# Kernel tuning notes

Hardware: AMD Instinct MI355X
Metric: run time of the kernel (lower is better)

The kernel has to match this reference:

```python
import jax, jax.numpy as jnp
import numpy as np

B, S, F = 256, 512, 26
H, M, C = 512, 256, 20  # rnn_hidden, mlp_hidden, num_classes


def setup_inputs() -> dict:
    key = jax.random.key(0)
    ks = jax.random.split(key, 9)
    s_ih = 1.0 / np.sqrt(H)
    return {
        "x": jax.random.normal(ks[0], (B, S, F), dtype=jnp.float32),
        "w_ih": jax.random.uniform(ks[1], (4 * H, F), jnp.float32, -s_ih, s_ih),
        "w_hh": jax.random.uniform(ks[2], (4 * H, H), jnp.float32, -s_ih, s_ih),
        "b_ih": jax.random.uniform(ks[3], (4 * H,), jnp.float32, -s_ih, s_ih),
        "b_hh": jax.random.uniform(ks[4], (4 * H,), jnp.float32, -s_ih, s_ih),
        "w1": jax.random.uniform(ks[5], (M, H), jnp.float32, -s_ih, s_ih),
        "b1": jax.random.uniform(ks[6], (M,), jnp.float32, -s_ih, s_ih),
        "w2": jax.random.uniform(ks[7], (C, M), jnp.float32, -1.0 / np.sqrt(M), 1.0 / np.sqrt(M)),
        "b2": jax.random.uniform(ks[8], (C,), jnp.float32, -1.0 / np.sqrt(M), 1.0 / np.sqrt(M)),
    }


def reference(x, w_ih, w_hh, b_ih, b_hh, w1, b1, w2, b2):
    b, s, _ = x.shape
    h0 = jnp.zeros((b, H), x.dtype)
    c0 = jnp.zeros((b, H), x.dtype)
    bias = b_ih + b_hh

    def step(carry, xt):
        h, c = carry
        # original stores hx.data -> state carried into next step is detached
        h = jax.lax.stop_gradient(h)
        c = jax.lax.stop_gradient(c)
        z = xt @ w_ih.T + h @ w_hh.T + bias  # [b, 4H]
        i, f, g, o = jnp.split(z, 4, axis=-1)  # PyTorch gate order i,f,g,o
        c2 = jax.nn.sigmoid(f) * c + jax.nn.sigmoid(i) * jnp.tanh(g)
        h2 = jax.nn.sigmoid(o) * jnp.tanh(c2)
        return (h2, c2), h2

    _, hs = jax.lax.scan(step, (h0, c0), jnp.transpose(x, (1, 0, 2)))  # hs: [s, b, H]
    hs = jnp.transpose(hs, (1, 0, 2))  # [b, s, H]
    hidden = jax.nn.relu(jnp.einsum("bsh,mh->bsm", hs, w1) + b1)
    logits = jnp.einsum("bsm,cm->bsc", hidden, w2) + b2
    return jax.nn.log_softmax(logits, axis=-1)
```

## Files before the change

kernel.cpp:

```cpp
#include <hip/hip_runtime.h>

#define S_LEN 512
#define HID   512
#define FEAT  26
#define NCLS  20
#define DRING 16

typedef short bf16x8 __attribute__((ext_vector_type(8)));
typedef float f32x4  __attribute__((ext_vector_type(4)));

__device__ __forceinline__ unsigned short f2bf(float f) {
    unsigned u = __builtin_bit_cast(unsigned, f);
    unsigned r = (u + 0x7FFFu + ((u >> 16) & 1u)) >> 16;
    return (unsigned short)r;
}
__device__ __forceinline__ float sigm(float x) { return 1.f / (1.f + __expf(-x)); }
__device__ __forceinline__ float tanh_f(float x) {
    float xc = fminf(fmaxf(x, -15.f), 15.f);
    float t = __expf(-2.f * xc);
    return (1.f - t) / (1.f + t);
}

__device__ __forceinline__ void load4_coherent(const unsigned short* p,
                                               uint4& a0, uint4& a1, uint4& a2, uint4& a3) {
    asm volatile(
        "global_load_dwordx4 %0, %4, off sc0 sc1\n\t"
        "global_load_dwordx4 %1, %5, off sc0 sc1\n\t"
        "global_load_dwordx4 %2, %6, off sc0 sc1\n\t"
        "global_load_dwordx4 %3, %7, off sc0 sc1\n\t"
        "s_waitcnt vmcnt(0)"
        : "=&v"(a0), "=&v"(a1), "=&v"(a2), "=&v"(a3)
        : "v"(p), "v"(p + 8), "v"(p + 16), "v"(p + 24)
        : "memory");
}
__device__ __forceinline__ void store_coherent(unsigned short* p, unsigned d) {
    asm volatile(
        "global_store_dword %0, %1, off sc0 sc1\n\t"
        "s_waitcnt vmcnt(0)"
        :: "v"(p), "v"(d) : "memory");
}
__device__ __forceinline__ void store_coherent_x2(unsigned short* p, unsigned long long d) {
    asm volatile(
        "global_store_dwordx2 %0, %1, off sc0 sc1\n\t"
        "s_waitcnt vmcnt(0)"
        :: "v"(p), "v"(d) : "memory");
}
__device__ __forceinline__ void store_u32_nowait(unsigned* p, unsigned d) {
    asm volatile("global_store_dword %0, %1, off sc0 sc1" :: "v"(p), "v"(d) : "memory");
}
__device__ __forceinline__ unsigned load_u32_coherent(const unsigned* p) {
    unsigned v;
    asm volatile("global_load_dword %0, %1, off sc0 sc1\n\ts_waitcnt vmcnt(0)"
                 : "=v"(v) : "v"(p) : "memory");
    return v;
}
__device__ __forceinline__ void store_u32_sys_wait(unsigned* p, unsigned d) {
    asm volatile("global_store_dword %0, %1, off sc0 sc1\n\ts_waitcnt vmcnt(0)"
                 :: "v"(p), "v"(d) : "memory");
}
__device__ __forceinline__ void load2_nw_sys(const unsigned short* p, uint4& a0, uint4& a1) {
    asm volatile(
        "global_load_dwordx4 %0, %2, off sc0 sc1\n\t"
        "global_load_dwordx4 %1, %3, off sc0 sc1"
        : "=&v"(a0), "=&v"(a1) : "v"(p), "v"(p + 8) : "memory");
}

__device__ __forceinline__ void load4_l2(const unsigned short* p,
                                         uint4& a0, uint4& a1, uint4& a2, uint4& a3) {
    asm volatile(
        "global_load_dwordx4 %0, %4, off sc0\n\t"
        "global_load_dwordx4 %1, %5, off sc0\n\t"
        "global_load_dwordx4 %2, %6, off sc0\n\t"
        "global_load_dwordx4 %3, %7, off sc0\n\t"
        "s_waitcnt vmcnt(0)"
        : "=&v"(a0), "=&v"(a1), "=&v"(a2), "=&v"(a3)
        : "v"(p), "v"(p + 8), "v"(p + 16), "v"(p + 24)
        : "memory");
}
__device__ __forceinline__ void store_l2_x2(unsigned short* p, unsigned long long d) {
    asm volatile(
        "global_store_dwordx2 %0, %1, off sc0\n\t"
        "s_waitcnt vmcnt(0)"
        :: "v"(p), "v"(d) : "memory");
}
__device__ __forceinline__ void store_u32_nowait_l2(unsigned* p, unsigned d) {
    asm volatile("global_store_dword %0, %1, off sc0" :: "v"(p), "v"(d) : "memory");
}
__device__ __forceinline__ unsigned load_u32_l2(const unsigned* p) {
    unsigned v;
    asm volatile("global_load_dword %0, %1, off sc0\n\ts_waitcnt vmcnt(0)"
                 : "=v"(v) : "v"(p) : "memory");
    return v;
}
__device__ __forceinline__ void load2_nw_l2(const unsigned short* p, uint4& a0, uint4& a1) {
    asm volatile(
        "global_load_dwordx4 %0, %2, off sc0\n\t"
        "global_load_dwordx4 %1, %3, off sc0"
        : "=&v"(a0), "=&v"(a1) : "v"(p), "v"(p + 8) : "memory");
}

__global__ void prep_kernel(const float* __restrict__ w1, const float* __restrict__ w2,
                            unsigned short* __restrict__ w1b, unsigned short* __restrict__ w2b,
                            unsigned* __restrict__ syncw, int nclear) {
    int i = blockIdx.x * 256 + threadIdx.x;
    if (i < nclear) syncw[i] = 0u;
    if (i < 256 * 512) w1b[i] = f2bf(w1[i]);
    if (i < NCLS * 256) w2b[i] = f2bf(w2[i]);
}

__global__ __launch_bounds__(256, 1) void lstm_big_kernel(
    const float* __restrict__ x,
    const float* __restrict__ w_ih,
    const float* __restrict__ w_hh,
    const float* __restrict__ b_ih,
    const float* __restrict__ b_hh,
    const unsigned short* __restrict__ w1b,
    const float* __restrict__ b1,
    const unsigned short* __restrict__ w2b,
    const float* __restrict__ b2,
    float* __restrict__ out,
    unsigned short* __restrict__ hs,
    unsigned* __restrict__ flags)
{
    const int tid  = threadIdx.x;
    const int wave = tid >> 6;
    const int lane = tid & 63;
    const int quad = lane >> 4;
    const int l16  = lane & 15;

    const int  bx      = blockIdx.x;
    const int  xasm    = bx & 7;
    const int  kslt    = bx >> 3;
    const bool is_lstm = (kslt < 16);
    const int  ksub    = is_lstm ? kslt : (kslt - 16);
    const int  clust   = xasm * 2 + (ksub >> 3);
    const int  sub     = ksub & 7;

    __shared__ __align__(16) unsigned short At[16 * 552];
    __shared__ __align__(16) unsigned short hid[16 * 264];
    __shared__ float lg[16 * 24];
    __shared__ unsigned rdy;
    __shared__ unsigned fastf;
    if (tid == 0) rdy = 0u;

    {
        unsigned xcc;
        asm volatile("s_getreg_b32 %0, hwreg(HW_REG_XCC_ID)" : "=s"(xcc));
        if (tid == 0) {
            unsigned* slot = flags + (clust * 8 + sub) * 16 + (is_lstm ? 8 : 9);
            store_u32_sys_wait(slot, (xcc & 0xFu) + 1u);
        }
        if (wave == 0) {
            const unsigned* ps = flags + (clust * 8 + (lane & 7)) * 16 + ((lane & 8) ? 9 : 8);
            unsigned myx = 1u;
            for (;;) {
                unsigned v = 1u;
                if (lane < 16) v = load_u32_coherent(ps);
                if (__ballot(v != 0u) == ~0ull) { myx = v; break; }
                __builtin_amdgcn_s_sleep(2);
            }
            unsigned ref = __shfl(myx, 0);
            bool eq = (lane >= 16) || (myx == ref);
            if (tid == 0) fastf = (__ballot(eq) == ~0ull) ? 1u : 0u;
        }
    }
    __syncthreads();
    const bool fast = (fastf != 0u);

    if (is_lstm) {
        const int wic = sub;
        const int B0  = clust * 16;
        const int U0  = wic * 64;

        bf16x8 bB[4][17];
#pragma unroll
        for (int g = 0; g < 4; ++g) {
            const int row = g * 512 + U0 + wave * 16 + l16;
            const float* wrow = w_hh + (size_t)row * HID;
#pragma unroll
            for (int kk = 0; kk < 16; ++kk) {
                const float* p = wrow + kk * 32 + quad * 8;
                bf16x8 v;
#pragma unroll
                for (int j = 0; j < 8; ++j) v[j] = (short)f2bf(p[j]);
                bB[g][kk] = v;
            }
            const float* irow = w_ih + (size_t)row * FEAT;
            bf16x8 v;
#pragma unroll
            for (int j = 0; j < 8; ++j) {
                int ftr = quad * 8 + j;
                v[j] = (ftr < FEAT) ? (short)f2bf(irow[ftr]) : (short)0;
            }
            bB[g][16] = v;
        }

        f32x4 biasv[4];
#pragma unroll
        for (int g = 0; g < 4; ++g)
#pragma unroll
            for (int r = 0; r < 4; ++r) {
                int rr = g * 512 + U0 + wave * 16 + quad * 4 + r;
                biasv[g][r] = b_ih[rr] + b_hh[rr];
            }
        float cst[4] = {0.f, 0.f, 0.f, 0.f};

        const int sm = tid >> 4;
        const int sc = tid & 15;
        unsigned short* hsc = hs + (size_t)clust * S_LEN * 16 * HID;
        unsigned* myflag = flags + (clust * 8 + wic) * 16;
        const unsigned* peer = flags + (clust * 8 + (lane & 7)) * 16;

        for (int t = 0; t < S_LEN; ++t) {
            {
                unsigned pk = 0u;
                if (sc <= 12) {
                    float2 xv = *(const float2*)(x + ((size_t)(B0 + sm) * S_LEN + t) * FEAT + sc * 2);
                    pk = (unsigned)f2bf(xv.x) | ((unsigned)f2bf(xv.y) << 16);
                }
                *(unsigned*)(At + sm * 552 + 512 + sc * 2) = pk;
            }

            f32x4 acc[4];
#pragma unroll
            for (int g = 0; g < 4; ++g) acc[g] = biasv[g];

            if (t > 0) {
                const unsigned tt = (unsigned)t;
                unsigned long long bal;
                for (;;) {
                    unsigned v = ~0u;
                    if (lane < 8) v = fast ? load_u32_l2(peer) : load_u32_coherent(peer);
                    bal = __ballot(v >= tt);
                    if ((bal & 0xFull) == 0xFull) break;
                    if (!fast) __builtin_amdgcn_s_sleep(1);
                }
                const bool g1ok = ((bal >> 4) & 0xFull) == 0xFull;

                const unsigned short* srow = hsc + ((size_t)(t - 1) * 16 + sm) * HID;
                uint4 s0, s1, s2, s3;
                if (fast) load2_nw_l2(srow + sc * 16, s0, s1);
                else      load2_nw_sys(srow + sc * 16, s0, s1);

                if (!g1ok) {
                    for (;;) {
                        unsigned v = ~0u;
                        if (lane >= 4 && lane < 8)
                            v = fast ? load_u32_l2(peer) : load_u32_coherent(peer);
                        unsigned long long b2_ = __ballot(v >= tt);
                        if (((b2_ >> 4) & 0xFull) == 0xFull) break;
                        if (!fast) __builtin_amdgcn_s_sleep(1);
                    }
                }
                asm volatile("s_waitcnt vmcnt(0)" ::: "memory");
                __builtin_amdgcn_sched_barrier(0);
                {
                    unsigned short* dst = At + sm * 552 + sc * 16;
                    *(uint4*)(dst)     = s0;
                    *(uint4*)(dst + 8) = s1;
                }
                if (fast) load2_nw_l2(srow + 256 + sc * 16, s2, s3);
                else      load2_nw_sys(srow + 256 + sc * 16, s2, s3);

                asm volatile("s_waitcnt lgkmcnt(0)" ::: "memory");
                __builtin_amdgcn_sched_barrier(0);
                __builtin_amdgcn_s_barrier();

                const unsigned short* arow = At + l16 * 552 + quad * 8;
                {
                    bf16x8 hx = __builtin_bit_cast(bf16x8, *(const uint4*)(arow + 16 * 32));
#pragma unroll
                    for (int g = 0; g < 4; ++g)
                        acc[g] = __builtin_amdgcn_mfma_f32_16x16x32_bf16(bB[g][16], hx, acc[g], 0, 0, 0);
                }
#pragma unroll
                for (int kk = 0; kk < 8; ++kk) {
                    bf16x8 h = __builtin_bit_cast(bf16x8, *(const uint4*)(arow + kk * 32));
#pragma unroll
                    for (int g = 0; g < 4; ++g)
                        acc[g] = __builtin_amdgcn_mfma_f32_16x16x32_bf16(bB[g][kk], h, acc[g], 0, 0, 0);
                }

                asm volatile("s_waitcnt vmcnt(0)" ::: "memory");
                __builtin_amdgcn_sched_barrier(0);
                {
                    unsigned short* dst = At + sm * 552 + 256 + sc * 16;
                    *(uint4*)(dst)     = s2;
                    *(uint4*)(dst + 8) = s3;
                }
                asm volatile("s_waitcnt lgkmcnt(0)" ::: "memory");
                __builtin_amdgcn_sched_barrier(0);
                __builtin_amdgcn_s_barrier();

#pragma unroll
                for (int kk = 8; kk < 16; ++kk) {
                    bf16x8 h = __builtin_bit_cast(bf16x8, *(const uint4*)(arow + kk * 32));
#pragma unroll
                    for (int g = 0; g < 4; ++g)
                        acc[g] = __builtin_amdgcn_mfma_f32_16x16x32_bf16(bB[g][kk], h, acc[g], 0, 0, 0);
                }
            } else {
                __syncthreads();
                const unsigned short* arow = At + l16 * 552 + quad * 8;
                bf16x8 hx = __builtin_bit_cast(bf16x8, *(const uint4*)(arow + 16 * 32));
#pragma unroll
                for (int g = 0; g < 4; ++g)
                    acc[g] = __builtin_amdgcn_mfma_f32_16x16x32_bf16(bB[g][16], hx, acc[g], 0, 0, 0);
            }

            {
                unsigned short hv[4];
#pragma unroll
                for (int r = 0; r < 4; ++r) {
                    float cn = sigm(acc[1][r]) * cst[r] + sigm(acc[0][r]) * tanh_f(acc[2][r]);
                    cst[r] = cn;
                    hv[r] = f2bf(sigm(acc[3][r]) * tanh_f(cn));
                }
                unsigned long long d = (unsigned long long)hv[0]
                                     | ((unsigned long long)hv[1] << 16)
                                     | ((unsigned long long)hv[2] << 32)
                                     | ((unsigned long long)hv[3] << 48);
                unsigned short* hp = hsc + ((size_t)t * 16 + l16) * HID
                                   + U0 + wave * 16 + quad * 4;
                if (fast) store_l2_x2(hp, d);
                else      store_coherent_x2(hp, d);
            }
            __syncthreads();
            if (tid == 0) {
                if (fast) store_u32_nowait_l2(myflag, (unsigned)(t + 1));
                else      store_u32_nowait(myflag, (unsigned)(t + 1));
            }
        }
    } else {
        const int mc  = clust;
        const int m   = sub;
        const int B0  = mc * 16;
        const unsigned* peer = flags + (mc * 8 + (lane & 7)) * 16;
        const unsigned short* hsc = hs + (size_t)mc * S_LEN * 16 * HID;
        const int sm = tid >> 4;
        const int sc = tid & 15;

        for (int t = m; t < S_LEN; t += 8) {
            if (wave == 0) {
                for (;;) {
                    unsigned v = fast ? load_u32_l2(peer) : load_u32_coherent(peer);
                    if (__ballot(v >= (unsigned)(t + 1)) == ~0ull) break;
                    __builtin_amdgcn_s_sleep(8);
                }
                if (lane == 0)
                    __hip_atomic_store(&rdy, (unsigned)(t + 1), __ATOMIC_RELAXED,
                                       __HIP_MEMORY_SCOPE_WORKGROUP);
            } else {
                while (__hip_atomic_load(&rdy, __ATOMIC_RELAXED,
                                         __HIP_MEMORY_SCOPE_WORKGROUP) < (unsigned)(t + 1))
                    __builtin_amdgcn_s_sleep(8);
            }
            {
                const unsigned short* src = hsc + ((size_t)t * 16 + sm) * HID + sc * 32;
                unsigned short* dst = At + sm * 552 + sc * 32;
                uint4 a0, a1, a2, a3;
                if (fast) load4_l2(src, a0, a1, a2, a3);
                else      load4_coherent(src, a0, a1, a2, a3);
                *(uint4*)(dst)      = a0;
                *(uint4*)(dst + 8)  = a1;
                *(uint4*)(dst + 16) = a2;
                *(uint4*)(dst + 24) = a3;
            }
            __syncthreads();

            f32x4 a1[4];
#pragma unroll
            for (int nt = 0; nt < 4; ++nt) a1[nt] = (f32x4){0.f, 0.f, 0.f, 0.f};
#pragma unroll
            for (int kk = 0; kk < 16; ++kk) {
                bf16x8 a = __builtin_bit_cast(
                    bf16x8, *(const uint4*)(At + l16 * 552 + kk * 32 + quad * 8));
#pragma unroll
                for (int nt = 0; nt < 4; ++nt) {
                    int n = wave * 64 + nt * 16 + l16;
                    bf16x8 b = __builtin_bit_cast(
                        bf16x8, *(const uint4*)(w1b + (size_t)n * 512 + kk * 32 + quad * 8));
                    a1[nt] = __builtin_amdgcn_mfma_f32_16x16x32_bf16(a, b, a1[nt], 0, 0, 0);
                }
            }
#pragma unroll
            for (int nt = 0; nt < 4; ++nt) {
                int n = wave * 64 + nt * 16 + l16;
                float bv = b1[n];
#pragma unroll
                for (int r = 0; r < 4; ++r)
                    hid[(quad * 4 + r) * 264 + n] = f2bf(fmaxf(a1[nt][r] + bv, 0.f));
            }
            __syncthreads();
            if (wave == 0) {
                f32x4 a2[2];
                a2[0] = (f32x4){0.f, 0.f, 0.f, 0.f};
                a2[1] = (f32x4){0.f, 0.f, 0.f, 0.f};
#pragma unroll
                for (int kk = 0; kk < 8; ++kk) {
                    bf16x8 a = __builtin_bit_cast(
                        bf16x8, *(const uint4*)(hid + l16 * 264 + kk * 32 + quad * 8));
#pragma unroll
                    for (int nt = 0; nt < 2; ++nt) {
                        int n = nt * 16 + l16;
                        bf16x8 b;
                        if (n < NCLS) {
                            b = __builtin_bit_cast(
                                bf16x8, *(const uint4*)(w2b + (size_t)n * 256 + kk * 32 + quad * 8));
                        } else {
                            uint4 z; z.x = z.y = z.z = z.w = 0u;
                            b = __builtin_bit_cast(bf16x8, z);
                        }
                        a2[nt] = __builtin_amdgcn_mfma_f32_16x16x32_bf16(a, b, a2[nt], 0, 0, 0);
                    }
                }
#pragma unroll
                for (int nt = 0; nt < 2; ++nt) {
                    int n = nt * 16 + l16;
                    if (n < NCLS) {
                        float bv = b2[n];
#pragma unroll
                        for (int r = 0; r < 4; ++r)
                            lg[(quad * 4 + r) * 24 + n] = a2[nt][r] + bv;
                    }
                }
            }
            __syncthreads();
            if (tid < 16) {
                float v[NCLS];
                float mx = -3.4e38f;
#pragma unroll
                for (int c = 0; c < NCLS; ++c) { v[c] = lg[tid * 24 + c]; mx = fmaxf(mx, v[c]); }
                float s = 0.f;
#pragma unroll
                for (int c = 0; c < NCLS; ++c) s += __expf(v[c] - mx);
                float lse = mx + __logf(s);
                float* orow = out + ((size_t)(B0 + tid) * S_LEN + t) * NCLS;
#pragma unroll
                for (int c = 0; c < NCLS; ++c) orow[c] = v[c] - lse;
            }
            __syncthreads();
        }
    }
}

__global__ __launch_bounds__(256, 2) void lstm_fused_kernel(
    const float* __restrict__ x, const float* __restrict__ w_ih,
    const float* __restrict__ w_hh, const float* __restrict__ b_ih,
    const float* __restrict__ b_hh, const unsigned short* __restrict__ w1b,
    const float* __restrict__ b1, const unsigned short* __restrict__ w2b,
    const float* __restrict__ b2, float* __restrict__ out,
    unsigned short* __restrict__ hb, unsigned* __restrict__ flags,
    unsigned* __restrict__ done)
{
    const int tid  = threadIdx.x;
    const int wave = tid >> 6;
    const int lane = tid & 63;
    const int quad = lane >> 4;
    const int l16  = lane & 15;
    const int wg   = blockIdx.x;

    __shared__ __align__(16) unsigned short At[16 * 552];
    __shared__ float zb[16 * 132];
    __shared__ __align__(16) unsigned short hid[16 * 264];
    __shared__ float lg[16 * 24];
    __shared__ unsigned rdy;
    if (tid == 0) rdy = 0u;
    __syncthreads();

    if (wg < 256) {
        const int clust = (wg & 7) * 2 + (wg >= 128 ? 1 : 0);
        const int wic   = (wg >> 3) & 15;
        const int B0    = clust * 16;
        const int U0    = wic * 32;

        bf16x8 bB[2][17];
#pragma unroll
        for (int tl = 0; tl < 2; ++tl) {
            const int row = wave * 512 + U0 + tl * 16 + l16;
            const float* wrow = w_hh + (size_t)row * HID;
#pragma unroll
            for (int kk = 0; kk < 16; ++kk) {
                const float* p = wrow + kk * 32 + quad * 8;
                bf16x8 v;
#pragma unroll
                for (int j = 0; j < 8; ++j) v[j] = (short)f2bf(p[j]);
                bB[tl][kk] = v;
            }
            const float* irow = w_ih + (size_t)row * FEAT;
            bf16x8 v;
#pragma unroll
            for (int j = 0; j < 8; ++j) {
                int ftr = quad * 8 + j;
                v[j] = (ftr < FEAT) ? (short)f2bf(irow[ftr]) : (short)0;
            }
            bB[tl][16] = v;
        }

        const int gb = tid >> 4;
        const int gu = tid & 15;
        float bias[2][4];
#pragma unroll
        for (int uu = 0; uu < 2; ++uu)
#pragma unroll
            for (int g = 0; g < 4; ++g) {
                int r = g * 512 + U0 + 2 * gu + uu;
                bias[uu][g] = b_ih[r] + b_hh[r];
            }
        float cst[2] = {0.f, 0.f};

        const int sm = tid >> 4;
        const int sc = tid & 15;
        unsigned short* hbc = hb + (size_t)clust * DRING * 16 * HID;
        unsigned* myflag = flags + (clust * 16 + wic) * 16;
        const unsigned* peer = flags + (clust * 16 + (lane & 15)) * 16;

        for (int t = 0; t < S_LEN; ++t) {
            {
                unsigned pk = 0u;
                if (sc <= 12) {
                    float2 xv = *(const float2*)(x + ((size_t)(B0 + sm) * S_LEN + t) * FEAT + sc * 2);
                    pk = (unsigned)f2bf(xv.x) | ((unsigned)f2bf(xv.y) << 16);
                }
                *(unsigned*)(At + sm * 552 + 512 + sc * 2) = pk;
            }
            if (t > 0) {
                if (wave == 0) {
                    if (t >= DRING && lane == 0) {
                        const unsigned* dn = done + (clust * 8 + (t & 7)) * 16;
                        while (load_u32_coherent(dn) < (unsigned)(t - (DRING - 1)))
                            __builtin_amdgcn_s_sleep(8);
                    }
                    for (;;) {
                        unsigned v = load_u32_coherent(peer);
                        if (__ballot(v >= (unsigned)t) == ~0ull) break;
                        __builtin_amdgcn_s_sleep(1);
                    }
                    if (lane == 0)
                        __hip_atomic_store(&rdy, (unsigned)t, __ATOMIC_RELAXED,
                                           __HIP_MEMORY_SCOPE_WORKGROUP);
                } else {
                    while (__hip_atomic_load(&rdy, __ATOMIC_RELAXED,
                                             __HIP_MEMORY_SCOPE_WORKGROUP) < (unsigned)t)
                        __builtin_amdgcn_s_sleep(1);
                }
                const unsigned short* src =
                    hbc + ((t - 1) & (DRING - 1)) * 16 * HID + sm * HID + sc * 32;
                unsigned short* dst = At + sm * 552 + sc * 32;
                uint4 a0, a1, a2, a3;
                load4_coherent(src, a0, a1, a2, a3);
                *(uint4*)(dst)      = a0;
                *(uint4*)(dst + 8)  = a1;
                *(uint4*)(dst + 16) = a2;
                *(uint4*)(dst + 24) = a3;
            }
            __syncthreads();

            f32x4 acc0 = {0.f, 0.f, 0.f, 0.f};
            f32x4 acc1 = {0.f, 0.f, 0.f, 0.f};
            const unsigned short* arow = At + l16 * 552 + quad * 8;
            if (t > 0) {
#pragma unroll
                for (int kk = 0; kk < 17; ++kk) {
                    bf16x8 a = __builtin_bit_cast(bf16x8, *(const uint4*)(arow + kk * 32));
                    acc0 = __builtin_amdgcn_mfma_f32_16x16x32_bf16(a, bB[0][kk], acc0, 0, 0, 0);
                    acc1 = __builtin_amdgcn_mfma_f32_16x16x32_bf16(a, bB[1][kk], acc1, 0, 0, 0);
                }
            } else {
                bf16x8 a = __builtin_bit_cast(bf16x8, *(const uint4*)(arow + 16 * 32));
                acc0 = __builtin_amdgcn_mfma_f32_16x16x32_bf16(a, bB[0][16], acc0, 0, 0, 0);
                acc1 = __builtin_amdgcn_mfma_f32_16x16x32_bf16(a, bB[1][16], acc1, 0, 0, 0);
            }
#pragma unroll
            for (int r = 0; r < 4; ++r) {
                zb[(quad * 4 + r) * 132 + wave * 32 + l16]      = acc0[r];
                zb[(quad * 4 + r) * 132 + wave * 32 + 16 + l16] = acc1[r];
            }
            __syncthreads();

            {
                const float* zrow = zb + gb * 132;
                unsigned short hv2[2];
#pragma unroll
                for (int uu = 0; uu < 2; ++uu) {
                    int u = 2 * gu + uu;
                    float zi = zrow[u]      + bias[uu][0];
                    float zf = zrow[32 + u] + bias[uu][1];
                    float zg = zrow[64 + u] + bias[uu][2];
                    float zo = zrow[96 + u] + bias[uu][3];
                    float cn = sigm(zf) * cst[uu] + sigm(zi) * tanh_f(zg);
                    cst[uu] = cn;
                    hv2[uu] = f2bf(sigm(zo) * tanh_f(cn));
                }
                unsigned short* hp =
                    hbc + (t & (DRING - 1)) * 16 * HID + gb * HID + U0 + 2 * gu;
                store_coherent(hp, (unsigned)hv2[0] | ((unsigned)hv2[1] << 16));
            }
            __syncthreads();
            if (tid == 0) store_u32_nowait(myflag, (unsigned)(t + 1));
        }
    } else {
        const int mwg  = wg - 256;
        const int mc   = mwg >> 3;
        const int m    = mwg & 7;
        const int B0   = mc * 16;
        unsigned* mydone = done + (mc * 8 + m) * 16;
        const unsigned* peer = flags + (mc * 16 + (lane & 15)) * 16;
        const unsigned short* hbc = hb + (size_t)mc * DRING * 16 * HID;
        const int sm = tid >> 4;
        const int sc = tid & 15;

        for (int t = m; t < S_LEN; t += 8) {
            if (wave == 0) {
                for (;;) {
                    unsigned v = load_u32_coherent(peer);
                    if (__ballot(v >= (unsigned)(t + 1)) == ~0ull) break;
                    __builtin_amdgcn_s_sleep(8);
                }
                if (lane == 0)
                    __hip_atomic_store(&rdy, (unsigned)(t + 1), __ATOMIC_RELAXED,
                                       __HIP_MEMORY_SCOPE_WORKGROUP);
            } else {
                while (__hip_atomic_load(&rdy, __ATOMIC_RELAXED,
                                         __HIP_MEMORY_SCOPE_WORKGROUP) < (unsigned)(t + 1))
                    __builtin_amdgcn_s_sleep(8);
            }
            {
                const unsigned short* src =
                    hbc + (t & (DRING - 1)) * 16 * HID + sm * HID + sc * 32;
                unsigned short* dst = At + sm * 552 + sc * 32;
                uint4 a0, a1, a2, a3;
                load4_coherent(src, a0, a1, a2, a3);
                *(uint4*)(dst)      = a0;
                *(uint4*)(dst + 8)  = a1;
                *(uint4*)(dst + 16) = a2;
                *(uint4*)(dst + 24) = a3;
            }
            __syncthreads();
            if (tid == 0) store_u32_nowait(mydone, (unsigned)(t + 1));

            f32x4 a1[4];
#pragma unroll
            for (int nt = 0; nt < 4; ++nt) a1[nt] = (f32x4){0.f, 0.f, 0.f, 0.f};
#pragma unroll
            for (int kk = 0; kk < 16; ++kk) {
                bf16x8 a = __builtin_bit_cast(
                    bf16x8, *(const uint4*)(At + l16 * 552 + kk * 32 + quad * 8));
#pragma unroll
                for (int nt = 0; nt < 4; ++nt) {
                    int n = wave * 64 + nt * 16 + l16;
                    bf16x8 b = __builtin_bit_cast(
                        bf16x8, *(const uint4*)(w1b + (size_t)n * 512 + kk * 32 + quad * 8));
                    a1[nt] = __builtin_amdgcn_mfma_f32_16x16x32_bf16(a, b, a1[nt], 0, 0, 0);
                }
            }
#pragma unroll
            for (int nt = 0; nt < 4; ++nt) {
                int n = wave * 64 + nt * 16 + l16;
                float bv = b1[n];
#pragma unroll
                for (int r = 0; r < 4; ++r)
                    hid[(quad * 4 + r) * 264 + n] = f2bf(fmaxf(a1[nt][r] + bv, 0.f));
            }
            __syncthreads();
            if (wave == 0) {
                f32x4 a2[2];
                a2[0] = (f32x4){0.f, 0.f, 0.f, 0.f};
                a2[1] = (f32x4){0.f, 0.f, 0.f, 0.f};
#pragma unroll
                for (int kk = 0; kk < 8; ++kk) {
                    bf16x8 a = __builtin_bit_cast(
                        bf16x8, *(const uint4*)(hid + l16 * 264 + kk * 32 + quad * 8));
#pragma unroll
                    for (int nt = 0; nt < 2; ++nt) {
                        int n = nt * 16 + l16;
                        bf16x8 b;
                        if (n < NCLS) {
                            b = __builtin_bit_cast(
                                bf16x8, *(const uint4*)(w2b + (size_t)n * 256 + kk * 32 + quad * 8));
                        } else {
                            uint4 z; z.x = z.y = z.z = z.w = 0u;
                            b = __builtin_bit_cast(bf16x8, z);
                        }
                        a2[nt] = __builtin_amdgcn_mfma_f32_16x16x32_bf16(a, b, a2[nt], 0, 0, 0);
                    }
                }
#pragma unroll
                for (int nt = 0; nt < 2; ++nt) {
                    int n = nt * 16 + l16;
                    if (n < NCLS) {
                        float bv = b2[n];
#pragma unroll
                        for (int r = 0; r < 4; ++r)
                            lg[(quad * 4 + r) * 24 + n] = a2[nt][r] + bv;
                    }
                }
            }
            __syncthreads();
            if (tid < 16) {
                float v[NCLS];
                float mx = -3.4e38f;
#pragma unroll
                for (int c = 0; c < NCLS; ++c) { v[c] = lg[tid * 24 + c]; mx = fmaxf(mx, v[c]); }
                float s = 0.f;
#pragma unroll
                for (int c = 0; c < NCLS; ++c) s += __expf(v[c] - mx);
                float lse = mx + __logf(s);
                float* orow = out + ((size_t)(B0 + tid) * S_LEN + t) * NCLS;
#pragma unroll
                for (int c = 0; c < NCLS; ++c) orow[c] = v[c] - lse;
            }
            __syncthreads();
        }
    }
}

extern "C" void kernel_launch(void* const* d_in, const int* in_sizes, int n_in,
                              void* d_out, int out_size, void* d_ws, size_t ws_size,
                              hipStream_t stream) {
    const float* x    = (const float*)d_in[0];
    const float* w_ih = (const float*)d_in[1];
    const float* w_hh = (const float*)d_in[2];
    const float* b_ih = (const float*)d_in[3];
    const float* b_hh = (const float*)d_in[4];
    const float* w1   = (const float*)d_in[5];
    const float* b1   = (const float*)d_in[6];
    const float* w2   = (const float*)d_in[7];
    const float* b2   = (const float*)d_in[8];
    char* ws = (char*)d_ws;

    const size_t HS_BYTES = (size_t)16 * S_LEN * 16 * HID * 2;
    const size_t NEED_BIG = HS_BYTES + 8192 + 262144 + 10240;

    if (ws_size >= NEED_BIG) {
        unsigned short* hsb   = (unsigned short*)ws;
        unsigned*       flags = (unsigned*)(ws + HS_BYTES);
        unsigned short* w1b   = (unsigned short*)(ws + HS_BYTES + 8192);
        unsigned short* w2b   = (unsigned short*)(ws + HS_BYTES + 8192 + 262144);
        prep_kernel<<<512, 256, 0, stream>>>(w1, w2, w1b, w2b, flags, 2048);
        lstm_big_kernel<<<256, 256, 0, stream>>>(x, w_ih, w_hh, b_ih, b_hh,
                                                 w1b, b1, w2b, b2,
                                                 (float*)d_out, hsb, flags);
    } else {
        unsigned short* hb    = (unsigned short*)ws;
        unsigned*       flags = (unsigned*)(ws + 4194304);
        unsigned*       done  = (unsigned*)(ws + 4194304 + 16384);
        unsigned short* w1b   = (unsigned short*)(ws + 4194304 + 16384 + 8192);
        unsigned short* w2b   = (unsigned short*)(ws + 4194304 + 16384 + 8192 + 262144);
        prep_kernel<<<512, 256, 0, stream>>>(w1, w2, w1b, w2b, flags, 6144);
        lstm_fused_kernel<<<384, 256, 0, stream>>>(x, w_ih, w_hh, b_ih, b_hh,
                                                   w1b, b1, w2b, b2,
                                                   (float*)d_out, hb, flags, done);
    }
}
```

Before: 1.946 ms.

## Use per-wave completion flags and register-resident x prefetch in LSTM recurrence

```diff
diff --git a/kernel.cpp b/kernel.cpp
--- a/kernel.cpp
+++ b/kernel.cpp
@@ -209,16 +209,29 @@
         const int sc = tid & 15;
         unsigned short* hsc = hs + (size_t)clust * S_LEN * 16 * HID;
         unsigned* myflag = flags + (clust * 8 + wic) * 16;
-        const unsigned* peer = flags + (clust * 8 + (lane & 7)) * 16;
+        const unsigned* peer32 = flags + (clust * 8 + (lane >> 2)) * 16 + (lane & 3);
+        const float* xrow = x + (size_t)(B0 + l16) * S_LEN * FEAT;
+
+        float2 xq0, xq1, xq2, xq3;
+        {
+            const float* xp = xrow + quad * 8;
+            xq0 = *(const float2*)(xp);
+            if (quad < 3) {
+                xq1 = *(const float2*)(xp + 2);
+                xq2 = *(const float2*)(xp + 4);
+                xq3 = *(const float2*)(xp + 6);
+            }
+        }
 
         for (int t = 0; t < S_LEN; ++t) {
-            {
-                unsigned pk = 0u;
-                if (sc <= 12) {
-                    float2 xv = *(const float2*)(x + ((size_t)(B0 + sm) * S_LEN + t) * FEAT + sc * 2);
-                    pk = (unsigned)f2bf(xv.x) | ((unsigned)f2bf(xv.y) << 16);
-                }
-                *(unsigned*)(At + sm * 552 + 512 + sc * 2) = pk;
+            bf16x8 xf;
+            xf[0] = (short)f2bf(xq0.x); xf[1] = (short)f2bf(xq0.y);
+            if (quad < 3) {
+                xf[2] = (short)f2bf(xq1.x); xf[3] = (short)f2bf(xq1.y);
+                xf[4] = (short)f2bf(xq2.x); xf[5] = (short)f2bf(xq2.y);
+                xf[6] = (short)f2bf(xq3.x); xf[7] = (short)f2bf(xq3.y);
+            } else {
+                xf[2] = 0; xf[3] = 0; xf[4] = 0; xf[5] = 0; xf[6] = 0; xf[7] = 0;
             }
 
             f32x4 acc[4];
@@ -230,25 +243,29 @@
                 unsigned long long bal;
                 for (;;) {
                     unsigned v = ~0u;
-                    if (lane < 8) v = fast ? load_u32_l2(peer) : load_u32_coherent(peer);
+                    if (lane < 32) v = fast ? load_u32_l2(peer32) : load_u32_coherent(peer32);
                     bal = __ballot(v >= tt);
-                    if ((bal & 0xFull) == 0xFull) break;
+                    if ((bal & 0xFFFFull) == 0xFFFFull) break;
                     if (!fast) __builtin_amdgcn_s_sleep(1);
                 }
-                const bool g1ok = ((bal >> 4) & 0xFull) == 0xFull;
+                const bool g1ok = ((bal >> 16) & 0xFFFFull) == 0xFFFFull;
 
                 const unsigned short* srow = hsc + ((size_t)(t - 1) * 16 + sm) * HID;
                 uint4 s0, s1, s2, s3;
                 if (fast) load2_nw_l2(srow + sc * 16, s0, s1);
                 else      load2_nw_sys(srow + sc * 16, s0, s1);
 
+#pragma unroll
+                for (int g = 0; g < 4; ++g)
+                    acc[g] = __builtin_amdgcn_mfma_f32_16x16x32_bf16(bB[g][16], xf, acc[g], 0, 0, 0);
+
                 if (!g1ok) {
                     for (;;) {
                         unsigned v = ~0u;
-                        if (lane >= 4 && lane < 8)
-                            v = fast ? load_u32_l2(peer) : load_u32_coherent(peer);
+                        if (lane >= 16 && lane < 32)
+                            v = fast ? load_u32_l2(peer32) : load_u32_coherent(peer32);
                         unsigned long long b2_ = __ballot(v >= tt);
-                        if (((b2_ >> 4) & 0xFull) == 0xFull) break;
+                        if (((b2_ >> 16) & 0xFFFFull) == 0xFFFFull) break;
                         if (!fast) __builtin_amdgcn_s_sleep(1);
                     }
                 }
@@ -267,12 +284,6 @@
                 __builtin_amdgcn_s_barrier();
 
                 const unsigned short* arow = At + l16 * 552 + quad * 8;
-                {
-                    bf16x8 hx = __builtin_bit_cast(bf16x8, *(const uint4*)(arow + 16 * 32));
-#pragma unroll
-                    for (int g = 0; g < 4; ++g)
-                        acc[g] = __builtin_amdgcn_mfma_f32_16x16x32_bf16(bB[g][16], hx, acc[g], 0, 0, 0);
-                }
 #pragma unroll
                 for (int kk = 0; kk < 8; ++kk) {
                     bf16x8 h = __builtin_bit_cast(bf16x8, *(const uint4*)(arow + kk * 32));
@@ -292,6 +303,16 @@
                 __builtin_amdgcn_sched_barrier(0);
                 __builtin_amdgcn_s_barrier();
 
+                if (t + 1 < S_LEN) {
+                    const float* xp = xrow + (size_t)(t + 1) * FEAT + quad * 8;
+                    xq0 = *(const float2*)(xp);
+                    if (quad < 3) {
+                        xq1 = *(const float2*)(xp + 2);
+                        xq2 = *(const float2*)(xp + 4);
+                        xq3 = *(const float2*)(xp + 6);
+                    }
+                }
+
 #pragma unroll
                 for (int kk = 8; kk < 16; ++kk) {
                     bf16x8 h = __builtin_bit_cast(bf16x8, *(const uint4*)(arow + kk * 32));
@@ -300,12 +321,18 @@
                         acc[g] = __builtin_amdgcn_mfma_f32_16x16x32_bf16(bB[g][kk], h, acc[g], 0, 0, 0);
                 }
             } else {
-                __syncthreads();
-                const unsigned short* arow = At + l16 * 552 + quad * 8;
-                bf16x8 hx = __builtin_bit_cast(bf16x8, *(const uint4*)(arow + 16 * 32));
 #pragma unroll
                 for (int g = 0; g < 4; ++g)
-                    acc[g] = __builtin_amdgcn_mfma_f32_16x16x32_bf16(bB[g][16], hx, acc[g], 0, 0, 0);
+                    acc[g] = __builtin_amdgcn_mfma_f32_16x16x32_bf16(bB[g][16], xf, acc[g], 0, 0, 0);
+                {
+                    const float* xp = xrow + (size_t)FEAT + quad * 8;
+                    xq0 = *(const float2*)(xp);
+                    if (quad < 3) {
+                        xq1 = *(const float2*)(xp + 2);
+                        xq2 = *(const float2*)(xp + 4);
+                        xq3 = *(const float2*)(xp + 6);
+                    }
+                }
             }
 
             {
@@ -325,17 +352,18 @@
                 if (fast) store_l2_x2(hp, d);
                 else      store_coherent_x2(hp, d);
             }
-            __syncthreads();
-            if (tid == 0) {
-                if (fast) store_u32_nowait_l2(myflag, (unsigned)(t + 1));
-                else      store_u32_nowait(myflag, (unsigned)(t + 1));
-            }
+            if (lane == 0) {
+                if (fast) store_u32_nowait_l2(myflag + wave, (unsigned)(t + 1));
+                else      store_u32_nowait(myflag + wave, (unsigned)(t + 1));
+            }
+            asm volatile("s_waitcnt lgkmcnt(0)" ::: "memory");
+            __builtin_amdgcn_s_barrier();
         }
     } else {
         const int mc  = clust;
         const int m   = sub;
         const int B0  = mc * 16;
-        const unsigned* peer = flags + (mc * 8 + (lane & 7)) * 16;
+        const unsigned* peer32 = flags + (mc * 8 + (lane >> 2)) * 16 + (lane & 3);
         const unsigned short* hsc = hs + (size_t)mc * S_LEN * 16 * HID;
         const int sm = tid >> 4;
         const int sc = tid & 15;
@@ -343,7 +371,8 @@
         for (int t = m; t < S_LEN; t += 8) {
             if (wave == 0) {
                 for (;;) {
-                    unsigned v = fast ? load_u32_l2(peer) : load_u32_coherent(peer);
+                    unsigned v = ~0u;
+                    if (lane < 32) v = fast ? load_u32_l2(peer32) : load_u32_coherent(peer32);
                     if (__ballot(v >= (unsigned)(t + 1)) == ~0ull) break;
                     __builtin_amdgcn_s_sleep(8);
                 }
```

Result: slower. 2.164 ms (+11.2%).

## Replace per-block flag with per-wave flags, polled as one 16-byte load

Applied to the files above, without the earlier changes.

```diff
diff --git a/kernel.cpp b/kernel.cpp
--- a/kernel.cpp
+++ b/kernel.cpp
@@ -64,6 +64,12 @@
         "global_load_dwordx4 %1, %3, off sc0 sc1"
         : "=&v"(a0), "=&v"(a1) : "v"(p), "v"(p + 8) : "memory");
 }
+__device__ __forceinline__ uint4 load_flags4_sys(const unsigned* p) {
+    uint4 v;
+    asm volatile("global_load_dwordx4 %0, %1, off sc0 sc1\n\ts_waitcnt vmcnt(0)"
+                 : "=v"(v) : "v"(p) : "memory");
+    return v;
+}
 
 __device__ __forceinline__ void load4_l2(const unsigned short* p,
                                          uint4& a0, uint4& a1, uint4& a2, uint4& a3) {
@@ -97,6 +103,17 @@
         "global_load_dwordx4 %0, %2, off sc0\n\t"
         "global_load_dwordx4 %1, %3, off sc0"
         : "=&v"(a0), "=&v"(a1) : "v"(p), "v"(p + 8) : "memory");
+}
+__device__ __forceinline__ uint4 load_flags4_l2(const unsigned* p) {
+    uint4 v;
+    asm volatile("global_load_dwordx4 %0, %1, off sc0\n\ts_waitcnt vmcnt(0)"
+                 : "=v"(v) : "v"(p) : "memory");
+    return v;
+}
+__device__ __forceinline__ unsigned min4u(uint4 f) {
+    unsigned a = f.x < f.y ? f.x : f.y;
+    unsigned b = f.z < f.w ? f.z : f.w;
+    return a < b ? a : b;
 }
 
 __global__ void prep_kernel(const float* __restrict__ w1, const float* __restrict__ w2,
@@ -209,7 +226,7 @@
         const int sc = tid & 15;
         unsigned short* hsc = hs + (size_t)clust * S_LEN * 16 * HID;
         unsigned* myflag = flags + (clust * 8 + wic) * 16;
-        const unsigned* peer = flags + (clust * 8 + (lane & 7)) * 16;
+        const unsigned* peerq = flags + (clust * 8 + (lane & 7)) * 16;
 
         for (int t = 0; t < S_LEN; ++t) {
             {
@@ -230,7 +247,10 @@
                 unsigned long long bal;
                 for (;;) {
                     unsigned v = ~0u;
-                    if (lane < 8) v = fast ? load_u32_l2(peer) : load_u32_coherent(peer);
+                    if (lane < 8) {
+                        uint4 f4 = fast ? load_flags4_l2(peerq) : load_flags4_sys(peerq);
+                        v = min4u(f4);
+                    }
                     bal = __ballot(v >= tt);
                     if ((bal & 0xFull) == 0xFull) break;
                     if (!fast) __builtin_amdgcn_s_sleep(1);
@@ -245,8 +265,10 @@
                 if (!g1ok) {
                     for (;;) {
                         unsigned v = ~0u;
-                        if (lane >= 4 && lane < 8)
-                            v = fast ? load_u32_l2(peer) : load_u32_coherent(peer);
+                        if (lane >= 4 && lane < 8) {
+                            uint4 f4 = fast ? load_flags4_l2(peerq) : load_flags4_sys(peerq);
+                            v = min4u(f4);
+                        }
                         unsigned long long b2_ = __ballot(v >= tt);
                         if (((b2_ >> 4) & 0xFull) == 0xFull) break;
                         if (!fast) __builtin_amdgcn_s_sleep(1);
@@ -325,17 +347,18 @@
                 if (fast) store_l2_x2(hp, d);
                 else      store_coherent_x2(hp, d);
             }
-            __syncthreads();
-            if (tid == 0) {
-                if (fast) store_u32_nowait_l2(myflag, (unsigned)(t + 1));
-                else      store_u32_nowait(myflag, (unsigned)(t + 1));
-            }
+            if (lane == 0) {
+                if (fast) store_u32_nowait_l2(myflag + wave, (unsigned)(t + 1));
+                else      store_u32_nowait(myflag + wave, (unsigned)(t + 1));
+            }
+            asm volatile("s_waitcnt lgkmcnt(0)" ::: "memory");
+            __builtin_amdgcn_s_barrier();
         }
     } else {
         const int mc  = clust;
         const int m   = sub;
         const int B0  = mc * 16;
-        const unsigned* peer = flags + (mc * 8 + (lane & 7)) * 16;
+        const unsigned* peerq = flags + (mc * 8 + (lane & 7)) * 16;
         const unsigned short* hsc = hs + (size_t)mc * S_LEN * 16 * HID;
         const int sm = tid >> 4;
         const int sc = tid & 15;
@@ -343,7 +366,11 @@
         for (int t = m; t < S_LEN; t += 8) {
             if (wave == 0) {
                 for (;;) {
-                    unsigned v = fast ? load_u32_l2(peer) : load_u32_coherent(peer);
+                    unsigned v = ~0u;
+                    if (lane < 8) {
+                        uint4 f4 = fast ? load_flags4_l2(peerq) : load_flags4_sys(peerq);
+                        v = min4u(f4);
+                    }
                     if (__ballot(v >= (unsigned)(t + 1)) == ~0ull) break;
                     __builtin_amdgcn_s_sleep(8);
                 }
```

Result: slower. 2.185 ms (+12.3%).
